# Kernel tuning notes

Measured on AMD Instinct MI355X. Metric: run time of the kernel, lower is better.

## Reference

```python
import jax, jax.numpy as jnp
import numpy as np

NC, ND = 100000, 100000
E, L = 500000, 100000
HID, OUT = 128, 64
NH, HD = 4, 32
NL = 2


def setup_inputs() -> dict:
    key = jax.random.key(0)
    ks = jax.random.split(key, 16)
    f = jnp.float32
    s_lin = 1.0 / np.sqrt(HID)
    s_rel = 1.0 / np.sqrt(HD)
    return {
        "emb_C": jax.random.normal(ks[0], (NC, HID), f) * 0.1,
        "emb_D": jax.random.normal(ks[1], (ND, HID), f) * 0.1,
        "kW": jax.random.normal(ks[2], (NL, 2, HID, HID), f) * s_lin,
        "kb": jnp.zeros((NL, 2, HID), f),
        "qW": jax.random.normal(ks[3], (NL, 2, HID, HID), f) * s_lin,
        "qb": jnp.zeros((NL, 2, HID), f),
        "vW": jax.random.normal(ks[4], (NL, 2, HID, HID), f) * s_lin,
        "vb": jnp.zeros((NL, 2, HID), f),
        "aW": jax.random.normal(ks[5], (NL, 2, HID, HID), f) * s_lin,
        "ab": jnp.zeros((NL, 2, HID), f),
        "skip": jnp.ones((NL, 2), f),
        "arel": jax.random.normal(ks[6], (NL, 2, NH, HD, HD), f) * s_rel,
        "mrel": jax.random.normal(ks[7], (NL, 2, NH, HD, HD), f) * s_rel,
        "prel": jnp.ones((NL, 2, NH), f),
        "outW": jax.random.normal(ks[8], (2, HID, OUT), f) * s_lin,
        "outb": jnp.zeros((2, OUT), f),
        # edge_index for (Compound -> Disease) and reverse (Disease -> Compound)
        "ei_cd": jnp.stack([jax.random.randint(ks[9], (E,), 0, NC),
                            jax.random.randint(ks[10], (E,), 0, ND)]).astype(jnp.int32),
        "ei_dc": jnp.stack([jax.random.randint(ks[11], (E,), 0, ND),
                            jax.random.randint(ks[12], (E,), 0, NC)]).astype(jnp.int32),
        # edge_label_index: (Compound, Disease) pairs to score
        "eli": jnp.stack([jax.random.randint(ks[13], (L,), 0, NC),
                          jax.random.randint(ks[14], (L,), 0, ND)]).astype(jnp.int32),
    }


def _seg_softmax(a, seg, n):
    # numerically stable softmax over edges grouped by destination node
    amax = jax.ops.segment_max(a, seg, num_segments=n)
    amax = jnp.where(jnp.isfinite(amax), amax, 0.0)
    ex = jnp.exp(a - amax[seg])
    den = jax.ops.segment_sum(ex, seg, num_segments=n)
    return ex / (den[seg] + 1e-16)


def _hgt_layer(xs, p, ei_cd, ei_dc):
    kW, kb, qW, qb, vW, vb, aW, ab, skip, arel, mrel, prel = p
    # per-node-type K/Q/V projections, reshaped to [N, heads, head_dim]
    k = [(xs[t] @ kW[t] + kb[t]).reshape(-1, NH, HD) for t in range(2)]
    q = [(xs[t] @ qW[t] + qb[t]).reshape(-1, NH, HD) for t in range(2)]
    v = [(xs[t] @ vW[t] + vb[t]).reshape(-1, NH, HD) for t in range(2)]
    outs = [jnp.zeros_like(k[0]), jnp.zeros_like(k[1])]
    rels = [(0, 1, ei_cd), (1, 0, ei_dc)]  # (src_type, dst_type, edge_index)
    for r, (s, d, ei) in enumerate(rels):
        # relation-specific transforms applied per source node (as in PyG HGTConv)
        krel = jnp.einsum('nhd,hde->nhe', k[s], arel[r])
        vrel = jnp.einsum('nhd,hde->nhe', v[s], mrel[r])
        src, dst = ei[0], ei[1]
        ndst = xs[d].shape[0]
        a = (q[d][dst] * krel[src]).sum(-1) * prel[r] / np.sqrt(HD)  # [E, NH]
        alpha = _seg_softmax(a, dst, ndst)
        msg = vrel[src] * alpha[..., None]                           # [E, NH, HD]
        outs[d] = outs[d] + jax.ops.segment_sum(msg, dst, num_segments=ndst)
    new = []
    for t in range(2):
        o = outs[t].reshape(-1, HID)
        o = jax.nn.gelu(o) @ aW[t] + ab[t]
        g = jax.nn.sigmoid(skip[t])
        new.append(g * o + (1.0 - g) * xs[t])  # skip connection (in==out dims)
    return new


def reference(emb_C, emb_D, kW, kb, qW, qb, vW, vb, aW, ab, skip, arel, mrel, prel,
              outW, outb, ei_cd, ei_dc, eli):
    xs = [emb_C, emb_D]
    for l in range(NL):
        p = (kW[l], kb[l], qW[l], qb[l], vW[l], vb[l], aW[l], ab[l],
             skip[l], arel[l], mrel[l], prel[l])
        xs = _hgt_layer(xs, p, ei_cd, ei_dc)
        xs = [jax.nn.relu(x) for x in xs]  # dropout(0.2) in eval mode -> identity
    zC = xs[0] @ outW[0] + outb[0]
    zD = xs[1] @ outW[1] + outb[1]
    logits = jnp.clip((zC[eli[0]] * zD[eli[1]]).sum(-1), -10.0, 10.0)
    return logits
```

## Files before the change

### kernel.cpp

```cpp
#include <hip/hip_runtime.h>
#include <math.h>

#define NC_   100000
#define ND_   100000
#define NN_   100000
#define E_CNT 500000
#define L_CNT 100000
#define NH_   4
#define HD_   32
#define WCAT_SZ (129 * 384)

typedef __attribute__((ext_vector_type(8))) short short8;
typedef __attribute__((ext_vector_type(4))) float floatx4;

__device__ __forceinline__ float gelu_f(float x) {
    const float c0 = 0.7978845608028654f;
    float x3 = x * x * x;
    return 0.5f * x * (1.0f + tanhf(c0 * (x + 0.044715f * x3)));
}

__device__ __forceinline__ unsigned short bf_rne(float x) {
    unsigned int u = __float_as_uint(x);
    u += 0x7fffu + ((u >> 16) & 1u);
    return (unsigned short)(u >> 16);
}
__device__ __forceinline__ float bf_to_f(unsigned short b) {
    return __uint_as_float(((unsigned int)b) << 16);
}

__device__ __forceinline__ void split3(const float* xv, short8* f) {
    #pragma unroll
    for (int i = 0; i < 8; i++) {
        float x = xv[i];
        unsigned short b0 = bf_rne(x);
        float x1 = x - bf_to_f(b0);
        unsigned short b1 = bf_rne(x1);
        float x2 = x1 - bf_to_f(b1);
        f[0][i] = (short)b0; f[1][i] = (short)b1; f[2][i] = (short)bf_rne(x2);
    }
}

__global__ __launch_bounds__(256) void fill0_int(int* __restrict__ p, int n) {
    int i = blockIdx.x * 256 + threadIdx.x;
    if (i < n) p[i] = 0;
}

__global__ __launch_bounds__(256) void count_dst(const int* __restrict__ dstA,
                                                 const int* __restrict__ dstB,
                                                 int* __restrict__ cnt) {
    int r = blockIdx.y;
    const int* dst = r ? dstB : dstA;
    int e = blockIdx.x * 256 + threadIdx.x;
    if (e < E_CNT) atomicAdd(&cnt[r * NN_ + dst[e]], 1);
}

__global__ __launch_bounds__(256) void scan_a(const int* __restrict__ cnt,
                                              int* __restrict__ excl,
                                              int* __restrict__ partials) {
    __shared__ int sd[256];
    int r = blockIdx.y;
    cnt += r * NN_; excl += r * (NN_ + 1); partials += r * 128;
    int b = blockIdx.x, t = threadIdx.x;
    int base = b * 1024 + t * 4;
    int v0 = (base + 0 < NN_) ? cnt[base + 0] : 0;
    int v1 = (base + 1 < NN_) ? cnt[base + 1] : 0;
    int v2 = (base + 2 < NN_) ? cnt[base + 2] : 0;
    int v3 = (base + 3 < NN_) ? cnt[base + 3] : 0;
    int tsum = v0 + v1 + v2 + v3;
    sd[t] = tsum; __syncthreads();
    for (int off = 1; off < 256; off <<= 1) {
        int x = (t >= off) ? sd[t - off] : 0;
        __syncthreads();
        sd[t] += x;
        __syncthreads();
    }
    int excl_t = sd[t] - tsum;
    if (t == 255) partials[b] = sd[t];
    int q = excl_t;
    if (base + 0 < NN_) excl[base + 0] = q; q += v0;
    if (base + 1 < NN_) excl[base + 1] = q; q += v1;
    if (base + 2 < NN_) excl[base + 2] = q; q += v2;
    if (base + 3 < NN_) excl[base + 3] = q;
}

__global__ __launch_bounds__(128) void scan_b(int* __restrict__ partials) {
    __shared__ int sd[128];
    partials += blockIdx.x * 128;
    int t = threadIdx.x;
    int orig = (t < 98) ? partials[t] : 0;
    sd[t] = orig; __syncthreads();
    for (int off = 1; off < 128; off <<= 1) {
        int x = (t >= off) ? sd[t - off] : 0;
        __syncthreads();
        sd[t] += x;
        __syncthreads();
    }
    if (t < 98) partials[t] = sd[t] - orig;
}

__global__ __launch_bounds__(256) void scan_c(int* __restrict__ row_ptr,
                                              const int* __restrict__ partials,
                                              int* __restrict__ cursor) {
    int r = blockIdx.y;
    row_ptr += r * (NN_ + 1); partials += r * 128; cursor += r * NN_;
    int b = blockIdx.x, t = threadIdx.x;
    int base = b * 1024 + t * 4;
    int add = partials[b];
    #pragma unroll
    for (int j = 0; j < 4; j++) {
        int i = base + j;
        if (i < NN_) { int v = row_ptr[i] + add; row_ptr[i] = v; cursor[i] = v; }
    }
    if (b == 0 && t == 0) row_ptr[NN_] = E_CNT;
}

__global__ __launch_bounds__(256) void scatter_edges(const int* __restrict__ srcA,
                                                     const int* __restrict__ dstA,
                                                     const int* __restrict__ srcB,
                                                     const int* __restrict__ dstB,
                                                     int* __restrict__ cursor,
                                                     int* __restrict__ srcs) {
    int r = blockIdx.y;
    const int* src = r ? srcB : srcA;
    const int* dst = r ? dstB : dstA;
    cursor += r * NN_; srcs += r * E_CNT;
    int e = blockIdx.x * 256 + threadIdx.x;
    if (e >= E_CNT) return;
    int pos = atomicAdd(&cursor[dst[e]], 1);
    srcs[pos] = src[e];
}

__global__ void fuse_weights(const float* __restrict__ qW, const float* __restrict__ qb,
                             const float* __restrict__ kW, const float* __restrict__ kb,
                             const float* __restrict__ vW, const float* __restrict__ vb,
                             const float* __restrict__ arel, const float* __restrict__ mrel,
                             float* __restrict__ WcatAll)
{
    int i  = blockIdx.x;
    int t  = blockIdx.y;
    int lyr = blockIdx.z;
    int oc = threadIdx.x;
    int lt = lyr * 2 + t;
    float* Wcat = WcatAll + (size_t)lt * WCAT_SZ;
    float val;
    if (oc < 128) {
        val = (i < 128) ? qW[(size_t)(lt * 128 + i) * 128 + oc] : qb[lt * 128 + oc];
    } else {
        int which = (oc >= 256);
        int cc = oc - (which ? 256 : 128);
        int h = cc >> 5, e = cc & 31;
        const float* W = which ? vW : kW;
        const float* b = which ? vb : kb;
        const float* R = (which ? mrel : arel) + (size_t)(lt * NH_ + h) * HD_ * HD_ + e;
        float s = 0.f;
        if (i < 128) {
            const float* wrow = W + (size_t)(lt * 128 + i) * 128 + h * 32;
            #pragma unroll
            for (int d2 = 0; d2 < 32; d2++) s += wrow[d2] * R[d2 * 32];
        } else {
            const float* brow = b + lt * 128 + h * 32;
            #pragma unroll
            for (int d2 = 0; d2 < 32; d2++) s += brow[d2] * R[d2 * 32];
        }
        val = s;
    }
    Wcat[(size_t)((i < 128) ? i : 128) * 384 + oc] = val;
}

__global__ __launch_bounds__(256)
void pack_w(const float* __restrict__ W, int ldw, int matStride,
            unsigned short* __restrict__ out, int N, int outMatStride)
{
    int mat = blockIdx.y;
    int e = blockIdx.x * 256 + threadIdx.x;
    int total = N * 16;
    if (e >= total) return;
    int lane = e & 63;
    int s = (e >> 6) & 3;
    int nt = e >> 8;
    int col = nt * 16 + (lane & 15);
    int k0 = s * 32 + ((lane >> 4) << 3);
    const float* src = W + (size_t)mat * matStride + (size_t)k0 * ldw + col;
    int ps = N * 128;
    unsigned short* o = out + (size_t)mat * outMatStride + (size_t)e * 8;
    short8 p0, p1, p2;
    #pragma unroll
    for (int j = 0; j < 8; j++) {
        float x = src[(size_t)j * ldw];
        unsigned short b0 = bf_rne(x);
        float x1 = x - bf_to_f(b0);
        unsigned short b1 = bf_rne(x1);
        float x2 = x1 - bf_to_f(b1);
        unsigned short b2 = bf_rne(x2);
        p0[j] = (short)b0; p1[j] = (short)b1; p2[j] = (short)b2;
    }
    *(short8*)(o)          = p0;
    *(short8*)(o + ps)     = p1;
    *(short8*)(o + 2 * ps) = p2;
}

template<int POST>
__global__ __launch_bounds__(256, 3)
void gemm_mfma(const float* __restrict__ A, int lda,
               const unsigned short* __restrict__ Bp, int pstride,
               const float* __restrict__ bias,
               float* __restrict__ C, int ldc, int M,
               const float* __restrict__ resid, const float* __restrict__ skipv,
               int ySplit,
               const float* __restrict__ A2, const unsigned short* __restrict__ Bp2,
               int pstride2, const float* __restrict__ bias2,
               float* __restrict__ C2, int ldc2)
{
    __shared__ unsigned short Blds[3 * 8192];
    int by = blockIdx.y;
    if (ySplit >= 0 && by >= ySplit) {
        A = A2; Bp = Bp2; pstride = pstride2; bias = bias2; C = C2; ldc = ldc2;
        by -= ySplit;
    }
    int tid  = threadIdx.x;
    int wave = tid >> 6, lane = tid & 63;
    int quad = lane >> 4, l16 = lane & 15;
    int bm = blockIdx.x * 128;
    int bn = by * 64;

    {
        const unsigned short* slab = Bp + (size_t)(bn >> 4) * 2048;
        #pragma unroll
        for (int p = 0; p < 3; p++) {
            const uint4* src = (const uint4*)(slab + (size_t)p * pstride);
            uint4* dst = (uint4*)&Blds[p * 8192];
            #pragma unroll
            for (int i = 0; i < 4; i++) dst[i * 256 + tid] = src[i * 256 + tid];
        }
    }

    int row0 = bm + wave * 32 + l16;
    int crow0 = min(row0, M - 1);
    int crow1 = min(row0 + 16, M - 1);
    const float* ap0 = A + (size_t)crow0 * lda + quad * 8;
    const float* ap1 = A + (size_t)crow1 * lda + quad * 8;

    float4 ar[2][2][2];
    ar[0][0][0] = *(const float4*)(ap0);
    ar[0][0][1] = *(const float4*)(ap0 + 4);
    ar[0][1][0] = *(const float4*)(ap1);
    ar[0][1][1] = *(const float4*)(ap1 + 4);

    floatx4 acc[2][4];
    #pragma unroll
    for (int m = 0; m < 2; m++)
        #pragma unroll
        for (int ct = 0; ct < 4; ct++) acc[m][ct] = (floatx4){0.f, 0.f, 0.f, 0.f};

    __syncthreads();

    constexpr int PA[6] = {0, 1, 2, 0, 1, 0};
    constexpr int PB[6] = {2, 1, 0, 1, 0, 0};

    #pragma unroll
    for (int s = 0; s < 4; s++) {
        const int cur = s & 1, nxt = cur ^ 1;
        if (s < 3) {
            ar[nxt][0][0] = *(const float4*)(ap0 + (s + 1) * 32);
            ar[nxt][0][1] = *(const float4*)(ap0 + (s + 1) * 32 + 4);
            ar[nxt][1][0] = *(const float4*)(ap1 + (s + 1) * 32);
            ar[nxt][1][1] = *(const float4*)(ap1 + (s + 1) * 32 + 4);
        }
        __builtin_amdgcn_sched_barrier(0);
        short8 bfr[4][3];
        #pragma unroll
        for (int ct = 0; ct < 4; ct++)
            #pragma unroll
            for (int p = 0; p < 3; p++)
                bfr[ct][p] = *(const short8*)&Blds[p * 8192 + ct * 2048 + s * 512 + lane * 8];
        short8 af0[3], af1[3];
        {
            float xv[8];
            *(float4*)&xv[0] = ar[cur][0][0]; *(float4*)&xv[4] = ar[cur][0][1];
            split3(xv, af0);
        }
        {
            float xv[8];
            *(float4*)&xv[0] = ar[cur][1][0]; *(float4*)&xv[4] = ar[cur][1][1];
            split3(xv, af1);
        }
        #pragma unroll
        for (int o = 0; o < 6; o++) {
            #pragma unroll
            for (int ct = 0; ct < 4; ct++) {
                acc[0][ct] = __builtin_amdgcn_mfma_f32_16x16x32_bf16(
                    af0[PA[o]], bfr[ct][PB[o]], acc[0][ct], 0, 0, 0);
                acc[1][ct] = __builtin_amdgcn_mfma_f32_16x16x32_bf16(
                    af1[PA[o]], bfr[ct][PB[o]], acc[1][ct], 0, 0, 0);
            }
        }
    }

    float g = 0.f, omg = 0.f;
    if (POST) { float sv = skipv[0]; g = 1.0f / (1.0f + expf(-sv)); omg = 1.0f - g; }
    #pragma unroll
    for (int m = 0; m < 2; m++) {
        #pragma unroll
        for (int ct = 0; ct < 4; ct++) {
            int col = bn + ct * 16 + l16;
            float bv = bias[col];
            #pragma unroll
            for (int i = 0; i < 4; i++) {
                int r = bm + wave * 32 + m * 16 + quad * 4 + i;
                if (r < M) {
                    float v = acc[m][ct][i] + bv;
                    if (POST) {
                        float rr = resid[(size_t)r * ldc + col];
                        v = fmaxf(g * v + omg * rr, 0.f);
                    }
                    C[(size_t)r * ldc + col] = v;
                }
            }
        }
    }
}

__global__ __launch_bounds__(256)
void attn_gather(const int* __restrict__ row_ptr, const int* __restrict__ srcs,
                 float* __restrict__ qo, const float* __restrict__ kv,
                 const float* __restrict__ prel, int ndst)
{
    int wave = (blockIdx.x * 256 + threadIdx.x) >> 6;
    int lane = threadIdx.x & 63;
    if (wave >= ndst) return;
    int d = wave;
    int gl = lane & 15;
    int group = lane >> 4;
    int h = gl >> 2;
    float pr = prel[h] * 0.17677669529663687f;
    int beg = row_ptr[d], end = row_ptr[d + 1];
    const float* qrow = qo + (size_t)d * 128 + gl * 8;
    float4 q0 = *(const float4*)(qrow);
    float4 q1 = *(const float4*)(qrow + 4);
    float m = -1.0e30f, l = 0.f;
    float4 acc0 = make_float4(0.f,0.f,0.f,0.f), acc1 = acc0;
    int nt = (end - beg + 3) >> 2;
    for (int t = 0; t < nt; t++) {
        int i = beg + (t << 2) + group;
        if (i < end) {
            int s = srcs[i];
            const float* row = kv + (size_t)s * 256 + gl * 8;
            float4 k0 = *(const float4*)(row);
            float4 k1 = *(const float4*)(row + 4);
            float4 v0 = *(const float4*)(row + 128);
            float4 v1 = *(const float4*)(row + 132);
            float part = q0.x*k0.x + q0.y*k0.y + q0.z*k0.z + q0.w*k0.w
                       + q1.x*k1.x + q1.y*k1.y + q1.z*k1.z + q1.w*k1.w;
            part += __shfl_xor(part, 1);
            part += __shfl_xor(part, 2);
            float a = part * pr;
            float mn = fmaxf(m, a);
            float scale = expf(m - mn);
            float p = expf(a - mn);
            l = l * scale + p;
            acc0.x = acc0.x * scale + p * v0.x;
            acc0.y = acc0.y * scale + p * v0.y;
            acc0.z = acc0.z * scale + p * v0.z;
            acc0.w = acc0.w * scale + p * v0.w;
            acc1.x = acc1.x * scale + p * v1.x;
            acc1.y = acc1.y * scale + p * v1.y;
            acc1.z = acc1.z * scale + p * v1.z;
            acc1.w = acc1.w * scale + p * v1.w;
            m = mn;
        }
    }
    #pragma unroll
    for (int mask = 16; mask <= 32; mask <<= 1) {
        float m_o = __shfl_xor(m, mask);
        float l_o = __shfl_xor(l, mask);
        float4 a0o, a1o;
        a0o.x = __shfl_xor(acc0.x, mask); a0o.y = __shfl_xor(acc0.y, mask);
        a0o.z = __shfl_xor(acc0.z, mask); a0o.w = __shfl_xor(acc0.w, mask);
        a1o.x = __shfl_xor(acc1.x, mask); a1o.y = __shfl_xor(acc1.y, mask);
        a1o.z = __shfl_xor(acc1.z, mask); a1o.w = __shfl_xor(acc1.w, mask);
        float mn = fmaxf(m, m_o);
        float s0 = expf(m - mn), s1 = expf(m_o - mn);
        l = l * s0 + l_o * s1;
        acc0.x = acc0.x * s0 + a0o.x * s1; acc0.y = acc0.y * s0 + a0o.y * s1;
        acc0.z = acc0.z * s0 + a0o.z * s1; acc0.w = acc0.w * s0 + a0o.w * s1;
        acc1.x = acc1.x * s0 + a1o.x * s1; acc1.y = acc1.y * s0 + a1o.y * s1;
        acc1.z = acc1.z * s0 + a1o.z * s1; acc1.w = acc1.w * s0 + a1o.w * s1;
        m = mn;
    }
    float inv = (beg == end) ? 0.f : 1.f / (l + 1e-16f);
    if (group == 0) {
        float* orow = qo + (size_t)d * 128 + gl * 8;
        float4 o0, o1;
        o0.x = gelu_f(acc0.x * inv); o0.y = gelu_f(acc0.y * inv);
        o0.z = gelu_f(acc0.z * inv); o0.w = gelu_f(acc0.w * inv);
        o1.x = gelu_f(acc1.x * inv); o1.y = gelu_f(acc1.y * inv);
        o1.z = gelu_f(acc1.z * inv); o1.w = gelu_f(acc1.w * inv);
        *(float4*)(orow)     = o0;
        *(float4*)(orow + 4) = o1;
    }
}

__global__ __launch_bounds__(256)
void score_pairs(const int* __restrict__ ic, const int* __restrict__ id,
                 const float* __restrict__ zC, const float* __restrict__ zD,
                 float* __restrict__ out)
{
    int gid = blockIdx.x * 256 + threadIdx.x;
    int p = gid >> 4, lane = gid & 15;
    if (p >= L_CNT) return;
    int c = ic[p], d = id[p];
    float4 a = *(const float4*)(zC + (size_t)c * 64 + lane * 4);
    float4 b = *(const float4*)(zD + (size_t)d * 64 + lane * 4);
    float s = a.x * b.x + a.y * b.y + a.z * b.z + a.w * b.w;
    s += __shfl_down(s, 8, 16);
    s += __shfl_down(s, 4, 16);
    s += __shfl_down(s, 2, 16);
    s += __shfl_down(s, 1, 16);
    if (lane == 0) out[p] = fminf(10.0f, fmaxf(-10.0f, s));
}

extern "C" void kernel_launch(void* const* d_in, const int* in_sizes, int n_in,
                              void* d_out, int out_size, void* d_ws, size_t ws_size,
                              hipStream_t stream)
{
    float* xC = (float*)d_in[0];
    float* xD = (float*)d_in[1];
    const float* kW   = (const float*)d_in[2];
    const float* kb   = (const float*)d_in[3];
    const float* qW   = (const float*)d_in[4];
    const float* qb   = (const float*)d_in[5];
    const float* vW   = (const float*)d_in[6];
    const float* vb   = (const float*)d_in[7];
    const float* aW   = (const float*)d_in[8];
    const float* ab   = (const float*)d_in[9];
    const float* skip = (const float*)d_in[10];
    const float* arel = (const float*)d_in[11];
    const float* mrel = (const float*)d_in[12];
    const float* prel = (const float*)d_in[13];
    const float* outW = (const float*)d_in[14];
    const float* outb = (const float*)d_in[15];
    const int* ei_cd  = (const int*)d_in[16];
    const int* ei_dc  = (const int*)d_in[17];
    const int* eli    = (const int*)d_in[18];

    float* ws = (float*)d_ws;
    size_t off = 0;
    float* kv    = ws + off; off += (size_t)NN_ * 256;
    float* qo    = ws + off; off += (size_t)NN_ * 128;
    float* Wcat  = ws + off; off += (size_t)4 * WCAT_SZ;
    unsigned short* WsCat = (unsigned short*)(ws + off); off += (4 * 3 * 384 * 128) / 2;
    unsigned short* aWs   = (unsigned short*)(ws + off); off += (4 * 3 * 128 * 128) / 2;
    unsigned short* outWs = (unsigned short*)(ws + off); off += (2 * 3 * 64 * 128) / 2;
    int* iws = (int*)(ws + off);
    size_t ioff = 0;
    int* rp      = iws + ioff; ioff += 2 * (NN_ + 1);
    int* srcsA   = iws + ioff; ioff += 2 * E_CNT;
    int* cnt     = iws + ioff; ioff += 2 * NN_;
    int* cursor  = iws + ioff; ioff += 2 * NN_;
    int* partial = iws + ioff; ioff += 256;
    float* zC = kv;
    float* zD = kv + (size_t)NN_ * 128;

    const int gridM = (NN_ + 127) / 128;
    const int gE    = (E_CNT + 255) / 256;
    const int gN2   = (2 * NN_ + 255) / 256;
    const int gScan = 98;
    const int gGath = (NN_ + 3) / 4;

    fill0_int<<<gN2, 256, 0, stream>>>(cnt, 2 * NN_);
    count_dst<<<dim3(gE, 2), 256, 0, stream>>>(ei_cd + E_CNT, ei_dc + E_CNT, cnt);
    scan_a<<<dim3(gScan, 2), 256, 0, stream>>>(cnt, rp, partial);
    scan_b<<<2, 128, 0, stream>>>(partial);
    scan_c<<<dim3(gScan, 2), 256, 0, stream>>>(rp, partial, cursor);
    scatter_edges<<<dim3(gE, 2), 256, 0, stream>>>(ei_cd, ei_cd + E_CNT,
                                                   ei_dc, ei_dc + E_CNT, cursor, srcsA);
    int* rp_cd   = rp;
    int* rp_dc   = rp + (NN_ + 1);
    int* srcs_cd = srcsA;
    int* srcs_dc = srcsA + E_CNT;

    fuse_weights<<<dim3(129, 2, 2), 384, 0, stream>>>(qW, qb, kW, kb, vW, vb,
                                                      arel, mrel, Wcat);
    pack_w<<<dim3((384 * 16 + 255) / 256, 4), 256, 0, stream>>>(
        Wcat, 384, WCAT_SZ, WsCat, 384, 3 * 384 * 128);
    pack_w<<<dim3((128 * 16 + 255) / 256, 4), 256, 0, stream>>>(
        aW, 128, 128 * 128, aWs, 128, 3 * 128 * 128);
    pack_w<<<dim3((64 * 16 + 255) / 256, 2), 256, 0, stream>>>(
        outW, 64, 128 * 64, outWs, 64, 3 * 64 * 128);

    const int PS_CAT = 384 * 128;
    const int PS_AW  = 128 * 128;
    const int PS_OW  = 64 * 128;

    for (int l = 0; l < 2; l++) {
        const float* abl = ab + (size_t)l * 2 * 128;
        float* WcC = Wcat + (size_t)(l * 2 + 0) * WCAT_SZ;
        float* WcD = Wcat + (size_t)(l * 2 + 1) * WCAT_SZ;
        const unsigned short* WsC = WsCat + (size_t)(l * 2 + 0) * 3 * PS_CAT;
        const unsigned short* WsD = WsCat + (size_t)(l * 2 + 1) * 3 * PS_CAT;
        const unsigned short* aWsD = aWs + (size_t)(l * 2 + 1) * 3 * PS_AW;
        const unsigned short* aWsC = aWs + (size_t)(l * 2 + 0) * 3 * PS_AW;

        gemm_mfma<0><<<dim3(gridM, 6), 256, 0, stream>>>(
            xC, 128, WsC + 128 * 128, PS_CAT, WcC + 128 * 384 + 128, kv, 256, NC_,
            nullptr, nullptr,
            4, xD, WsD, PS_CAT, WcD + 128 * 384, qo, 128);
        attn_gather<<<gGath, 256, 0, stream>>>(rp_cd, srcs_cd, qo, kv,
                                               prel + (l * 2 + 0) * 4, ND_);

        gemm_mfma<0><<<dim3(gridM, 4), 256, 0, stream>>>(
            xD, 128, WsD + 128 * 128, PS_CAT, WcD + 128 * 384 + 128, kv, 256, ND_,
            nullptr, nullptr, -1, nullptr, nullptr, 0, nullptr, nullptr, 0);

        gemm_mfma<1><<<dim3(gridM, 2), 256, 0, stream>>>(
            qo, 128, aWsD, PS_AW, abl + 128, xD, 128, ND_,
            xD, skip + l * 2 + 1, -1, nullptr, nullptr, 0, nullptr, nullptr, 0);

        gemm_mfma<0><<<dim3(gridM, 2), 256, 0, stream>>>(
            xC, 128, WsC, PS_CAT, WcC + 128 * 384, qo, 128, NC_,
            nullptr, nullptr, -1, nullptr, nullptr, 0, nullptr, nullptr, 0);
        attn_gather<<<gGath, 256, 0, stream>>>(rp_dc, srcs_dc, qo, kv,
                                               prel + (l * 2 + 1) * 4, NC_);

        gemm_mfma<1><<<dim3(gridM, 2), 256, 0, stream>>>(
            qo, 128, aWsC, PS_AW, abl, xC, 128, NC_,
            xC, skip + l * 2 + 0, -1, nullptr, nullptr, 0, nullptr, nullptr, 0);
    }

    gemm_mfma<0><<<dim3(gridM, 2), 256, 0, stream>>>(
        xC, 128, outWs, PS_OW, outb, zC, 64, NC_, nullptr, nullptr,
        1, xD, outWs + 3 * PS_OW, PS_OW, outb + 64, zD, 64);

    score_pairs<<<(L_CNT * 16 + 255) / 256, 256, 0, stream>>>(
        eli, eli + L_CNT, zC, zD, (float*)d_out);
}
```

Before: 1.212 ms.

## Enlarge GEMM tiles, truncate bf16 split, widen attention lanes per edge

The GEMM blocks grow to 512 threads covering 256 rows, so each LDS-staged weight slab is reused across twice as many rows. The three-way bf16 split of A switches from round-to-nearest to truncation, which cuts ALU work per element while keeping the exact three-term residual decomposition. The attention gather gives each lane 16 features so that 8 edges are processed per wave iteration instead of 4, raising memory-level parallelism on the irregular K/V loads. In exchange, register pressure rises in both kernels and the larger GEMM blocks reduce the number of blocks available for load balancing.

```diff
diff --git a/kernel.cpp b/kernel.cpp
--- a/kernel.cpp
+++ b/kernel.cpp
@@ -28,15 +28,17 @@
     return __uint_as_float(((unsigned int)b) << 16);
 }
 
-__device__ __forceinline__ void split3(const float* xv, short8* f) {
+__device__ __forceinline__ void split3t(const float* xv, short8* f) {
     #pragma unroll
     for (int i = 0; i < 8; i++) {
-        float x = xv[i];
-        unsigned short b0 = bf_rne(x);
-        float x1 = x - bf_to_f(b0);
-        unsigned short b1 = bf_rne(x1);
-        float x2 = x1 - bf_to_f(b1);
-        f[0][i] = (short)b0; f[1][i] = (short)b1; f[2][i] = (short)bf_rne(x2);
+        unsigned int u0 = __float_as_uint(xv[i]);
+        float r1 = xv[i] - __uint_as_float(u0 & 0xFFFF0000u);
+        unsigned int u1 = __float_as_uint(r1);
+        float r2 = r1 - __uint_as_float(u1 & 0xFFFF0000u);
+        unsigned int u2 = __float_as_uint(r2);
+        f[0][i] = (short)(u0 >> 16);
+        f[1][i] = (short)(u1 >> 16);
+        f[2][i] = (short)(u2 >> 16);
     }
 }
 
@@ -200,7 +202,7 @@
 }
 
 template<int POST>
-__global__ __launch_bounds__(256, 3)
+__global__ __launch_bounds__(512, 4)
 void gemm_mfma(const float* __restrict__ A, int lda,
                const unsigned short* __restrict__ Bp, int pstride,
                const float* __restrict__ bias,
@@ -220,7 +222,7 @@
     int tid  = threadIdx.x;
     int wave = tid >> 6, lane = tid & 63;
     int quad = lane >> 4, l16 = lane & 15;
-    int bm = blockIdx.x * 128;
+    int bm = blockIdx.x * 256;
     int bn = by * 64;
 
     {
@@ -230,7 +232,7 @@
             const uint4* src = (const uint4*)(slab + (size_t)p * pstride);
             uint4* dst = (uint4*)&Blds[p * 8192];
             #pragma unroll
-            for (int i = 0; i < 4; i++) dst[i * 256 + tid] = src[i * 256 + tid];
+            for (int i = 0; i < 2; i++) dst[i * 512 + tid] = src[i * 512 + tid];
         }
     }
 
@@ -277,12 +279,12 @@
         {
             float xv[8];
             *(float4*)&xv[0] = ar[cur][0][0]; *(float4*)&xv[4] = ar[cur][0][1];
-            split3(xv, af0);
+            split3t(xv, af0);
         }
         {
             float xv[8];
             *(float4*)&xv[0] = ar[cur][1][0]; *(float4*)&xv[4] = ar[cur][1][1];
-            split3(xv, af1);
+            split3t(xv, af1);
         }
         #pragma unroll
         for (int o = 0; o < 6; o++) {
@@ -329,74 +331,95 @@
     int lane = threadIdx.x & 63;
     if (wave >= ndst) return;
     int d = wave;
-    int gl = lane & 15;
-    int group = lane >> 4;
-    int h = gl >> 2;
+    int gl = lane & 7;
+    int group = lane >> 3;
+    int h = gl >> 1;
     float pr = prel[h] * 0.17677669529663687f;
     int beg = row_ptr[d], end = row_ptr[d + 1];
-    const float* qrow = qo + (size_t)d * 128 + gl * 8;
+    const float* qrow = qo + (size_t)d * 128 + gl * 16;
     float4 q0 = *(const float4*)(qrow);
     float4 q1 = *(const float4*)(qrow + 4);
+    float4 q2 = *(const float4*)(qrow + 8);
+    float4 q3 = *(const float4*)(qrow + 12);
     float m = -1.0e30f, l = 0.f;
-    float4 acc0 = make_float4(0.f,0.f,0.f,0.f), acc1 = acc0;
-    int nt = (end - beg + 3) >> 2;
+    float4 a0 = make_float4(0.f,0.f,0.f,0.f), a1 = a0, a2 = a0, a3 = a0;
+    int nt = (end - beg + 7) >> 3;
     for (int t = 0; t < nt; t++) {
-        int i = beg + (t << 2) + group;
+        int i = beg + (t << 3) + group;
         if (i < end) {
             int s = srcs[i];
-            const float* row = kv + (size_t)s * 256 + gl * 8;
+            const float* row = kv + (size_t)s * 256 + gl * 16;
             float4 k0 = *(const float4*)(row);
             float4 k1 = *(const float4*)(row + 4);
+            float4 k2 = *(const float4*)(row + 8);
+            float4 k3 = *(const float4*)(row + 12);
             float4 v0 = *(const float4*)(row + 128);
             float4 v1 = *(const float4*)(row + 132);
+            float4 v2 = *(const float4*)(row + 136);
+            float4 v3 = *(const float4*)(row + 140);
             float part = q0.x*k0.x + q0.y*k0.y + q0.z*k0.z + q0.w*k0.w
-                       + q1.x*k1.x + q1.y*k1.y + q1.z*k1.z + q1.w*k1.w;
+                       + q1.x*k1.x + q1.y*k1.y + q1.z*k1.z + q1.w*k1.w
+                       + q2.x*k2.x + q2.y*k2.y + q2.z*k2.z + q2.w*k2.w
+                       + q3.x*k3.x + q3.y*k3.y + q3.z*k3.z + q3.w*k3.w;
             part += __shfl_xor(part, 1);
-            part += __shfl_xor(part, 2);
             float a = part * pr;
             float mn = fmaxf(m, a);
             float scale = expf(m - mn);
             float p = expf(a - mn);
             l = l * scale + p;
-            acc0.x = acc0.x * scale + p * v0.x;
-            acc0.y = acc0.y * scale + p * v0.y;
-            acc0.z = acc0.z * scale + p * v0.z;
-            acc0.w = acc0.w * scale + p * v0.w;
-            acc1.x = acc1.x * scale + p * v1.x;
-            acc1.y = acc1.y * scale + p * v1.y;
-            acc1.z = acc1.z * scale + p * v1.z;
-            acc1.w = acc1.w * scale + p * v1.w;
+            a0.x = a0.x * scale + p * v0.x; a0.y = a0.y * scale + p * v0.y;
+            a0.z = a0.z * scale + p * v0.z; a0.w = a0.w * scale + p * v0.w;
+            a1.x = a1.x * scale + p * v1.x; a1.y = a1.y * scale + p * v1.y;
+            a1.z = a1.z * scale + p * v1.z; a1.w = a1.w * scale + p * v1.w;
+            a2.x = a2.x * scale + p * v2.x; a2.y = a2.y * scale + p * v2.y;
+            a2.z = a2.z * scale + p * v2.z; a2.w = a2.w * scale + p * v2.w;
+            a3.x = a3.x * scale + p * v3.x; a3.y = a3.y * scale + p * v3.y;
+            a3.z = a3.z * scale + p * v3.z; a3.w = a3.w * scale + p * v3.w;
             m = mn;
         }
     }
     #pragma unroll
-    for (int mask = 16; mask <= 32; mask <<= 1) {
+    for (int mask = 8; mask <= 32; mask <<= 1) {
         float m_o = __shfl_xor(m, mask);
         float l_o = __shfl_xor(l, mask);
-        float4 a0o, a1o;
-        a0o.x = __shfl_xor(acc0.x, mask); a0o.y = __shfl_xor(acc0.y, mask);
-        a0o.z = __shfl_xor(acc0.z, mask); a0o.w = __shfl_xor(acc0.w, mask);
-        a1o.x = __shfl_xor(acc1.x, mask); a1o.y = __shfl_xor(acc1.y, mask);
-        a1o.z = __shfl_xor(acc1.z, mask); a1o.w = __shfl_xor(acc1.w, mask);
+        float4 b0, b1, b2, b3;
+        b0.x = __shfl_xor(a0.x, mask); b0.y = __shfl_xor(a0.y, mask);
+        b0.z = __shfl_xor(a0.z, mask); b0.w = __shfl_xor(a0.w, mask);
+        b1.x = __shfl_xor(a1.x, mask); b1.y = __shfl_xor(a1.y, mask);
+        b1.z = __shfl_xor(a1.z, mask); b1.w = __shfl_xor(a1.w, mask);
+        b2.x = __shfl_xor(a2.x, mask); b2.y = __shfl_xor(a2.y, mask);
+        b2.z = __shfl_xor(a2.z, mask); b2.w = __shfl_xor(a2.w, mask);
+        b3.x = __shfl_xor(a3.x, mask); b3.y = __shfl_xor(a3.y, mask);
+        b3.z = __shfl_xor(a3.z, mask); b3.w = __shfl_xor(a3.w, mask);
         float mn = fmaxf(m, m_o);
         float s0 = expf(m - mn), s1 = expf(m_o - mn);
         l = l * s0 + l_o * s1;
-        acc0.x = acc0.x * s0 + a0o.x * s1; acc0.y = acc0.y * s0 + a0o.y * s1;
-        acc0.z = acc0.z * s0 + a0o.z * s1; acc0.w = acc0.w * s0 + a0o.w * s1;
-        acc1.x = acc1.x * s0 + a1o.x * s1; acc1.y = acc1.y * s0 + a1o.y * s1;
-        acc1.z = acc1.z * s0 + a1o.z * s1; acc1.w = acc1.w * s0 + a1o.w * s1;
+        a0.x = a0.x * s0 + b0.x * s1; a0.y = a0.y * s0 + b0.y * s1;
+        a0.z = a0.z * s0 + b0.z * s1; a0.w = a0.w * s0 + b0.w * s1;
+        a1.x = a1.x * s0 + b1.x * s1; a1.y = a1.y * s0 + b1.y * s1;
+        a1.z = a1.z * s0 + b1.z * s1; a1.w = a1.w * s0 + b1.w * s1;
+        a2.x = a2.x * s0 + b2.x * s1; a2.y = a2.y * s0 + b2.y * s1;
+        a2.z = a2.z * s0 + b2.z * s1; a2.w = a2.w * s0 + b2.w * s1;
+        a3.x = a3.x * s0 + b3.x * s1; a3.y = a3.y * s0 + b3.y * s1;
+        a3.z = a3.z * s0 + b3.z * s1; a3.w = a3.w * s0 + b3.w * s1;
         m = mn;
     }
     float inv = (beg == end) ? 0.f : 1.f / (l + 1e-16f);
     if (group == 0) {
-        float* orow = qo + (size_t)d * 128 + gl * 8;
-        float4 o0, o1;
-        o0.x = gelu_f(acc0.x * inv); o0.y = gelu_f(acc0.y * inv);
-        o0.z = gelu_f(acc0.z * inv); o0.w = gelu_f(acc0.w * inv);
-        o1.x = gelu_f(acc1.x * inv); o1.y = gelu_f(acc1.y * inv);
-        o1.z = gelu_f(acc1.z * inv); o1.w = gelu_f(acc1.w * inv);
-        *(float4*)(orow)     = o0;
-        *(float4*)(orow + 4) = o1;
+        float* orow = qo + (size_t)d * 128 + gl * 16;
+        float4 o0, o1, o2, o3;
+        o0.x = gelu_f(a0.x * inv); o0.y = gelu_f(a0.y * inv);
+        o0.z = gelu_f(a0.z * inv); o0.w = gelu_f(a0.w * inv);
+        o1.x = gelu_f(a1.x * inv); o1.y = gelu_f(a1.y * inv);
+        o1.z = gelu_f(a1.z * inv); o1.w = gelu_f(a1.w * inv);
+        o2.x = gelu_f(a2.x * inv); o2.y = gelu_f(a2.y * inv);
+        o2.z = gelu_f(a2.z * inv); o2.w = gelu_f(a2.w * inv);
+        o3.x = gelu_f(a3.x * inv); o3.y = gelu_f(a3.y * inv);
+        o3.z = gelu_f(a3.z * inv); o3.w = gelu_f(a3.w * inv);
+        *(float4*)(orow)      = o0;
+        *(float4*)(orow + 4)  = o1;
+        *(float4*)(orow + 8)  = o2;
+        *(float4*)(orow + 12) = o3;
     }
 }
 
@@ -461,7 +484,7 @@
     float* zC = kv;
     float* zD = kv + (size_t)NN_ * 128;
 
-    const int gridM = (NN_ + 127) / 128;
+    const int gridM = (NN_ + 255) / 256;
     const int gE    = (E_CNT + 255) / 256;
     const int gN2   = (2 * NN_ + 255) / 256;
     const int gScan = 98;
@@ -501,33 +524,33 @@
         const unsigned short* aWsD = aWs + (size_t)(l * 2 + 1) * 3 * PS_AW;
         const unsigned short* aWsC = aWs + (size_t)(l * 2 + 0) * 3 * PS_AW;
 
-        gemm_mfma<0><<<dim3(gridM, 6), 256, 0, stream>>>(
+        gemm_mfma<0><<<dim3(gridM, 6), 512, 0, stream>>>(
             xC, 128, WsC + 128 * 128, PS_CAT, WcC + 128 * 384 + 128, kv, 256, NC_,
             nullptr, nullptr,
             4, xD, WsD, PS_CAT, WcD + 128 * 384, qo, 128);
         attn_gather<<<gGath, 256, 0, stream>>>(rp_cd, srcs_cd, qo, kv,
                                                prel + (l * 2 + 0) * 4, ND_);
 
-        gemm_mfma<0><<<dim3(gridM, 4), 256, 0, stream>>>(
+        gemm_mfma<0><<<dim3(gridM, 4), 512, 0, stream>>>(
             xD, 128, WsD + 128 * 128, PS_CAT, WcD + 128 * 384 + 128, kv, 256, ND_,
             nullptr, nullptr, -1, nullptr, nullptr, 0, nullptr, nullptr, 0);
 
-        gemm_mfma<1><<<dim3(gridM, 2), 256, 0, stream>>>(
+        gemm_mfma<1><<<dim3(gridM, 2), 512, 0, stream>>>(
             qo, 128, aWsD, PS_AW, abl + 128, xD, 128, ND_,
             xD, skip + l * 2 + 1, -1, nullptr, nullptr, 0, nullptr, nullptr, 0);
 
-        gemm_mfma<0><<<dim3(gridM, 2), 256, 0, stream>>>(
+        gemm_mfma<0><<<dim3(gridM, 2), 512, 0, stream>>>(
             xC, 128, WsC, PS_CAT, WcC + 128 * 384, qo, 128, NC_,
             nullptr, nullptr, -1, nullptr, nullptr, 0, nullptr, nullptr, 0);
         attn_gather<<<gGath, 256, 0, stream>>>(rp_dc, srcs_dc, qo, kv,
                                                prel + (l * 2 + 1) * 4, NC_);
 
-        gemm_mfma<1><<<dim3(gridM, 2), 256, 0, stream>>>(
+        gemm_mfma<1><<<dim3(gridM, 2), 512, 0, stream>>>(
             qo, 128, aWsC, PS_AW, abl, xC, 128, NC_,
             xC, skip + l * 2 + 0, -1, nullptr, nullptr, 0, nullptr, nullptr, 0);
     }
 
-    gemm_mfma<0><<<dim3(gridM, 2), 256, 0, stream>>>(
+    gemm_mfma<0><<<dim3(gridM, 2), 512, 0, stream>>>(
         xC, 128, outWs, PS_OW, outb, zC, 64, NC_, nullptr, nullptr,
         1, xD, outWs + 3 * PS_OW, PS_OW, outb + 64, zD, 64);
 
```

After: 1.308 ms. +7.9%, slower.

## Enlarge GEMM blocks, truncate bf16 splits, use fast exp/rcp, spread gather epilogue

Applied to the files above, without the earlier changes.

The GEMM kernel now runs 512-thread blocks covering 256 rows each, so every staged B slab in LDS is reused by twice as many rows. The three-way bf16 split of A drops round-to-nearest-even in favour of plain truncation, which costs fewer ALU ops. Attention softmax and GELU switch to __expf and hardware reciprocal instead of expf, tanhf and division. The gather epilogue now has all four lane groups each write two outputs, rather than one group writing eight. Precision may shift slightly, and the larger blocks reduce the number of blocks available to fill the GPU.

```diff
diff --git a/kernel.cpp b/kernel.cpp
--- a/kernel.cpp
+++ b/kernel.cpp
@@ -15,8 +15,10 @@
 
 __device__ __forceinline__ float gelu_f(float x) {
     const float c0 = 0.7978845608028654f;
-    float x3 = x * x * x;
-    return 0.5f * x * (1.0f + tanhf(c0 * (x + 0.044715f * x3)));
+    float z = c0 * (x + 0.044715f * x * x * x);
+    float e = __expf(2.0f * z);
+    float t = 1.0f - 2.0f * __builtin_amdgcn_rcpf(e + 1.0f);
+    return 0.5f * x * (1.0f + t);
 }
 
 __device__ __forceinline__ unsigned short bf_rne(float x) {
@@ -28,15 +30,17 @@
     return __uint_as_float(((unsigned int)b) << 16);
 }
 
-__device__ __forceinline__ void split3(const float* xv, short8* f) {
+__device__ __forceinline__ void split3t(const float* xv, short8* f) {
     #pragma unroll
     for (int i = 0; i < 8; i++) {
-        float x = xv[i];
-        unsigned short b0 = bf_rne(x);
-        float x1 = x - bf_to_f(b0);
-        unsigned short b1 = bf_rne(x1);
-        float x2 = x1 - bf_to_f(b1);
-        f[0][i] = (short)b0; f[1][i] = (short)b1; f[2][i] = (short)bf_rne(x2);
+        unsigned int u0 = __float_as_uint(xv[i]);
+        float r1 = xv[i] - __uint_as_float(u0 & 0xFFFF0000u);
+        unsigned int u1 = __float_as_uint(r1);
+        float r2 = r1 - __uint_as_float(u1 & 0xFFFF0000u);
+        unsigned int u2 = __float_as_uint(r2);
+        f[0][i] = (short)(u0 >> 16);
+        f[1][i] = (short)(u1 >> 16);
+        f[2][i] = (short)(u2 >> 16);
     }
 }
 
@@ -200,7 +204,7 @@
 }
 
 template<int POST>
-__global__ __launch_bounds__(256, 3)
+__global__ __launch_bounds__(512, 4)
 void gemm_mfma(const float* __restrict__ A, int lda,
                const unsigned short* __restrict__ Bp, int pstride,
                const float* __restrict__ bias,
@@ -220,7 +224,7 @@
     int tid  = threadIdx.x;
     int wave = tid >> 6, lane = tid & 63;
     int quad = lane >> 4, l16 = lane & 15;
-    int bm = blockIdx.x * 128;
+    int bm = blockIdx.x * 256;
     int bn = by * 64;
 
     {
@@ -230,7 +234,7 @@
             const uint4* src = (const uint4*)(slab + (size_t)p * pstride);
             uint4* dst = (uint4*)&Blds[p * 8192];
             #pragma unroll
-            for (int i = 0; i < 4; i++) dst[i * 256 + tid] = src[i * 256 + tid];
+            for (int i = 0; i < 2; i++) dst[i * 512 + tid] = src[i * 512 + tid];
         }
     }
 
@@ -277,12 +281,12 @@
         {
             float xv[8];
             *(float4*)&xv[0] = ar[cur][0][0]; *(float4*)&xv[4] = ar[cur][0][1];
-            split3(xv, af0);
+            split3t(xv, af0);
         }
         {
             float xv[8];
             *(float4*)&xv[0] = ar[cur][1][0]; *(float4*)&xv[4] = ar[cur][1][1];
-            split3(xv, af1);
+            split3t(xv, af1);
         }
         #pragma unroll
         for (int o = 0; o < 6; o++) {
@@ -355,8 +359,8 @@
             part += __shfl_xor(part, 2);
             float a = part * pr;
             float mn = fmaxf(m, a);
-            float scale = expf(m - mn);
-            float p = expf(a - mn);
+            float scale = __expf(m - mn);
+            float p = __expf(a - mn);
             l = l * scale + p;
             acc0.x = acc0.x * scale + p * v0.x;
             acc0.y = acc0.y * scale + p * v0.y;
@@ -379,7 +383,7 @@
         a1o.x = __shfl_xor(acc1.x, mask); a1o.y = __shfl_xor(acc1.y, mask);
         a1o.z = __shfl_xor(acc1.z, mask); a1o.w = __shfl_xor(acc1.w, mask);
         float mn = fmaxf(m, m_o);
-        float s0 = expf(m - mn), s1 = expf(m_o - mn);
+        float s0 = __expf(m - mn), s1 = __expf(m_o - mn);
         l = l * s0 + l_o * s1;
         acc0.x = acc0.x * s0 + a0o.x * s1; acc0.y = acc0.y * s0 + a0o.y * s1;
         acc0.z = acc0.z * s0 + a0o.z * s1; acc0.w = acc0.w * s0 + a0o.w * s1;
@@ -387,17 +391,16 @@
         acc1.z = acc1.z * s0 + a1o.z * s1; acc1.w = acc1.w * s0 + a1o.w * s1;
         m = mn;
     }
-    float inv = (beg == end) ? 0.f : 1.f / (l + 1e-16f);
-    if (group == 0) {
-        float* orow = qo + (size_t)d * 128 + gl * 8;
-        float4 o0, o1;
-        o0.x = gelu_f(acc0.x * inv); o0.y = gelu_f(acc0.y * inv);
-        o0.z = gelu_f(acc0.z * inv); o0.w = gelu_f(acc0.w * inv);
-        o1.x = gelu_f(acc1.x * inv); o1.y = gelu_f(acc1.y * inv);
-        o1.z = gelu_f(acc1.z * inv); o1.w = gelu_f(acc1.w * inv);
-        *(float4*)(orow)     = o0;
-        *(float4*)(orow + 4) = o1;
-    }
+    float inv = (beg == end) ? 0.f : __builtin_amdgcn_rcpf(l + 1e-16f);
+    float s0v, s1v;
+    if (group == 0)      { s0v = acc0.x; s1v = acc0.y; }
+    else if (group == 1) { s0v = acc0.z; s1v = acc0.w; }
+    else if (group == 2) { s0v = acc1.x; s1v = acc1.y; }
+    else                 { s0v = acc1.z; s1v = acc1.w; }
+    float2 o;
+    o.x = gelu_f(s0v * inv);
+    o.y = gelu_f(s1v * inv);
+    *(float2*)(qo + (size_t)d * 128 + gl * 8 + group * 2) = o;
 }
 
 __global__ __launch_bounds__(256)
@@ -461,7 +464,7 @@
     float* zC = kv;
     float* zD = kv + (size_t)NN_ * 128;
 
-    const int gridM = (NN_ + 127) / 128;
+    const int gridM = (NN_ + 255) / 256;
     const int gE    = (E_CNT + 255) / 256;
     const int gN2   = (2 * NN_ + 255) / 256;
     const int gScan = 98;
@@ -501,33 +504,33 @@
         const unsigned short* aWsD = aWs + (size_t)(l * 2 + 1) * 3 * PS_AW;
         const unsigned short* aWsC = aWs + (size_t)(l * 2 + 0) * 3 * PS_AW;
 
-        gemm_mfma<0><<<dim3(gridM, 6), 256, 0, stream>>>(
+        gemm_mfma<0><<<dim3(gridM, 6), 512, 0, stream>>>(
             xC, 128, WsC + 128 * 128, PS_CAT, WcC + 128 * 384 + 128, kv, 256, NC_,
             nullptr, nullptr,
             4, xD, WsD, PS_CAT, WcD + 128 * 384, qo, 128);
         attn_gather<<<gGath, 256, 0, stream>>>(rp_cd, srcs_cd, qo, kv,
                                                prel + (l * 2 + 0) * 4, ND_);
 
-        gemm_mfma<0><<<dim3(gridM, 4), 256, 0, stream>>>(
+        gemm_mfma<0><<<dim3(gridM, 4), 512, 0, stream>>>(
             xD, 128, WsD + 128 * 128, PS_CAT, WcD + 128 * 384 + 128, kv, 256, ND_,
             nullptr, nullptr, -1, nullptr, nullptr, 0, nullptr, nullptr, 0);
 
-        gemm_mfma<1><<<dim3(gridM, 2), 256, 0, stream>>>(
+        gemm_mfma<1><<<dim3(gridM, 2), 512, 0, stream>>>(
             qo, 128, aWsD, PS_AW, abl + 128, xD, 128, ND_,
             xD, skip + l * 2 + 1, -1, nullptr, nullptr, 0, nullptr, nullptr, 0);
 
-        gemm_mfma<0><<<dim3(gridM, 2), 256, 0, stream>>>(
+        gemm_mfma<0><<<dim3(gridM, 2), 512, 0, stream>>>(
             xC, 128, WsC, PS_CAT, WcC + 128 * 384, qo, 128, NC_,
             nullptr, nullptr, -1, nullptr, nullptr, 0, nullptr, nullptr, 0);
         attn_gather<<<gGath, 256, 0, stream>>>(rp_dc, srcs_dc, qo, kv,
                                                prel + (l * 2 + 1) * 4, NC_);
 
-        gemm_mfma<1><<<dim3(gridM, 2), 256, 0, stream>>>(
+        gemm_mfma<1><<<dim3(gridM, 2), 512, 0, stream>>>(
             qo, 128, aWsC, PS_AW, abl, xC, 128, NC_,
             xC, skip + l * 2 + 0, -1, nullptr, nullptr, 0, nullptr, nullptr, 0);
     }
 
-    gemm_mfma<0><<<dim3(gridM, 2), 256, 0, stream>>>(
+    gemm_mfma<0><<<dim3(gridM, 2), 512, 0, stream>>>(
         xC, 128, outWs, PS_OW, outb, zC, 64, NC_, nullptr, nullptr,
         1, xD, outWs + 3 * PS_OW, PS_OW, outb + 64, zD, 64);
 
```

Result: no change. 1.197 ms (-1.2%).
